# Kernel optimization log

Hardware: AMD Instinct MI355X
Metric: run time of the kernel (lower is better)

Reference implementation:

```python
import jax, jax.numpy as jnp
import numpy as np
from jax.tree_util import tree_map

B, T, D = 2, 4096, 1024
C = 512            # chunk_size
P = 16             # n_persistent
H = 2048           # neural-memory hidden
FFN = 4 * D        # ffn_mult * d_model
LR, BETA, ALPHA = 0.01, 0.9, 0.01   # memory lr / momentum / decay
EPS_LN = 1e-5


def _l2norm(x):
    n = jnp.sqrt(jnp.sum(x * x, axis=-1, keepdims=True))
    return x / jnp.maximum(n, 1e-12)


def _ln(x, g, b):
    m = jnp.mean(x, axis=-1, keepdims=True)
    v = jnp.mean((x - m) ** 2, axis=-1, keepdims=True)
    return (x - m) * jax.lax.rsqrt(v + EPS_LN) * g + b


def _mem_mlp(mem, x):
    h = jax.nn.silu(x @ mem['w0'] + mem['b0'])
    return h @ mem['w1'] + mem['b1']


def setup_inputs() -> dict:
    key = jax.random.key(0)
    ks = iter(jax.random.split(key, 32))
    w = lambda *s: jax.random.normal(next(ks), s, jnp.float32) * 0.02
    return dict(
        x=jax.random.normal(next(ks), (B, T, D), jnp.float32),
        wq_ctx=w(D, D), wq=w(D, D), wk=w(D, D), wv=w(D, D),
        w_attn_out=w(D, D), w_gate=w(D, D),
        gate_g=jnp.ones(D), gate_b=jnp.zeros(D),
        n1_g=jnp.ones(D), n1_b=jnp.zeros(D),
        n2_g=jnp.ones(D), n2_b=jnp.zeros(D),
        ffn_w1=w(D, FFN), ffn_b1=jnp.zeros(FFN),
        ffn_w2=w(FFN, D), ffn_b2=jnp.zeros(D),
        pers=w(P, D),
        mem_w0=w(D, H), mem_b0=jnp.zeros(H),
        mem_w1=w(H, D), mem_b1=jnp.zeros(D),
        mem_wk=w(D, D), mem_wv=w(D, D),
    )


def reference(x, wq_ctx, wq, wk, wv, w_attn_out, w_gate, gate_g, gate_b,
              n1_g, n1_b, n2_g, n2_b, ffn_w1, ffn_b1, ffn_w2, ffn_b2,
              pers, mem_w0, mem_b0, mem_w1, mem_b1, mem_wk, mem_wv):
    Bv, Tv, Dv = x.shape
    n_chunks = Tv // C
    scale = Dv ** 0.5
    S = P + 2 * C   # persistent + retrieved-memory tokens + segment
    # prefix-aware causal mask: i attends to j if j < P (persistent prefix) or j <= i
    ii = jnp.arange(S)[:, None]
    jj = jnp.arange(S)[None, :]
    mask = (jj < P) | (jj <= ii)                      # (S, S)

    mem0 = dict(w0=mem_w0, b0=mem_b0, w1=mem_w1, b1=mem_b1)
    mom0 = tree_map(jnp.zeros_like, mem0)

    def attn(seq):                                    # cosine causal attention, single head
        q = _l2norm(seq @ wq) * scale
        k = _l2norm(seq @ wk)
        v = seq @ wv
        scores = jnp.einsum('bqd,bkd->bqk', q, k)
        scores = jnp.where(mask, scores, -jnp.inf)
        a = jax.nn.softmax(scores, axis=-1)
        return jnp.einsum('bqk,bkd->bqd', a, v) @ w_attn_out

    def step(carry, seg):                             # seg: (B, C, D)
        mem, mom = carry
        h = _mem_mlp(mem, _l2norm(seg @ wq_ctx))      # memory retrieval, (B, C, D)
        aug = jnp.concatenate(
            [jnp.broadcast_to(pers, (Bv, P, Dv)), h, seg], axis=1)  # (B, S, D)
        y_aug = aug + attn(_ln(aug, n1_g, n1_b))
        y_t = y_aug[:, P + C:, :]                     # strip persistent, keep last C

        # surprise-gradient memory update with momentum + decay
        kk = y_t @ mem_wk
        vv = y_t @ mem_wv
        loss = lambda m: 0.5 * jnp.sum((_mem_mlp(m, kk) - vv) ** 2) / (Bv * C)
        g = jax.grad(loss)(mem)
        mom = tree_map(lambda m_, g_: BETA * m_ + g_, mom, g)
        mem = tree_map(lambda p_, m_: (1.0 - ALPHA) * p_ - LR * m_, mem, mom)

        mem_out = _mem_mlp(mem, _l2norm(y_t @ wq_ctx))
        gate = jax.nn.sigmoid(_ln(y_t, gate_g, gate_b) @ w_gate)
        o = y_t * gate + mem_out * (1.0 - gate)
        h2 = _ln(o, n2_g, n2_b)
        o = o + (jax.nn.silu(h2 @ ffn_w1 + ffn_b1) @ ffn_w2 + ffn_b2)
        return (mem, mom), o

    x_chunks = x.reshape(Bv, n_chunks, C, Dv).transpose(1, 0, 2, 3)
    _, outs = jax.lax.scan(step, (mem0, mom0), x_chunks)   # (n_chunks, B, C, D)
    return outs.transpose(1, 0, 2, 3).reshape(Bv, Tv, Dv)
```

## Files before the change

kernel.cpp:

```cpp
#include <hip/hip_runtime.h>

#define DD 1024
#define HH 2048
#define TT 4096
#define CC 512
#define PPc 16
#define SB 1040
#define KA 1088
#define FFd 4096
#define NCH 8

typedef _Float16 f16x8 __attribute__((ext_vector_type(8)));
typedef float f32x4 __attribute__((ext_vector_type(4)));

typedef const __attribute__((address_space(1))) _Float16* gas_t;
typedef __attribute__((address_space(3))) _Float16* las_t;

__device__ __forceinline__ void async_cp16(const _Float16* g, _Float16* l) {
    __builtin_amdgcn_global_load_lds((gas_t)g, (las_t)l, 16, 0, 0);
}

template<int N> __device__ __forceinline__ void waitvm() {
    static_assert(N == 0 || N == 2 || N == 3 || N == 4 || N == 6 || N == 8, "unsupported vmcnt");
    if constexpr (N == 0)      asm volatile("s_waitcnt vmcnt(0)" ::: "memory");
    else if constexpr (N == 2) asm volatile("s_waitcnt vmcnt(2)" ::: "memory");
    else if constexpr (N == 3) asm volatile("s_waitcnt vmcnt(3)" ::: "memory");
    else if constexpr (N == 4) asm volatile("s_waitcnt vmcnt(4)" ::: "memory");
    else if constexpr (N == 6) asm volatile("s_waitcnt vmcnt(6)" ::: "memory");
    else                       asm volatile("s_waitcnt vmcnt(8)" ::: "memory");
}
#define BARRIER() asm volatile("s_barrier" ::: "memory")

struct GP {
    const _Float16* A; long bsA;
    const _Float16* Bt; long bsB;
    const float* bias;
    const float* resid; long ldr, bsR;
    const float* aux;   long ldx, bsX;
    float* Cf; long ldc, bsC;
    _Float16* Ch; long ldh, bsH;
    _Float16* Ct; long ldt, bsT;
    float* Mom;
    float* Cf2;
    float s1, s2;
    int M, N, K, act;
};

template<int BM, int BN>
__global__ __launch_bounds__(256) void gemm16(GP g)
{
    constexpr int WM = BM / 2, WN = BN / 2;
    constexpr int FA = WM / 16, FB = WN / 16;
    constexpr int LA = BM / 32, LB = BN / 32;
    constexpr int LL = LA + LB;
    constexpr int APAN = BM * 64, BPAN = BN * 64;
    constexpr int NB = 3;
    __shared__ _Float16 smem[NB * (APAN + BPAN)];
    const int tid = threadIdx.x;

    const int gx = gridDim.x, gy = gridDim.y;
    const int nwg = gx * gy * (int)gridDim.z;
    const int orig = ((int)blockIdx.z * gy + (int)blockIdx.y) * gx + (int)blockIdx.x;
    const int xcd = orig & 7, loc = orig >> 3;
    const int q8 = nwg >> 3, r8 = nwg & 7;
    const int lid = (xcd < r8 ? xcd * (q8 + 1) : r8 * (q8 + 1) + (xcd - r8) * q8) + loc;
    const int bxi = lid % gx;
    const int rem = lid / gx;
    const int byi = rem % gy;
    const int z = rem / gy;

    const int K = g.K;
    const int m0 = byi * BM, n0 = bxi * BN;
    const _Float16* Ab = g.A + (long)z * g.bsA + (long)m0 * K;
    const _Float16* Bb = g.Bt + (long)z * g.bsB + (long)n0 * K;
    const int wave = tid >> 6, lane = tid & 63;
    const int wr = wave >> 1, wc = wave & 1;
    const int fr = lane & 15, kq = lane >> 4;
    const int srow = tid >> 3;
    const int sc8 = (((tid & 7) ^ (srow & 7)) << 3);
    f32x4 acc[FA][FB] = {};

    auto stage = [&](int q, int kk) {
#pragma unroll
        for (int r = 0; r < LA; ++r)
            async_cp16(Ab + (long)(r * 32 + srow) * K + kk + sc8,
                       &smem[q * APAN + r * 2048 + wave * 512]);
#pragma unroll
        for (int r = 0; r < LB; ++r)
            async_cp16(Bb + (long)(r * 32 + srow) * K + kk + sc8,
                       &smem[NB * APAN + q * BPAN + r * 2048 + wave * 512]);
    };

    const int sl0 = ((kq ^ (fr & 7)) << 3);
    const int sl1 = (((4 + kq) ^ (fr & 7)) << 3);

    auto compute = [&](int q) {
        f16x8 af[2][FA], bf[2][FB];
        const int abase = q * APAN;
#pragma unroll
        for (int i = 0; i < FA; ++i) {
            const int ro = (wr * WM + i * 16 + fr) * 64;
            af[0][i] = *(const f16x8*)&smem[abase + ro + sl0];
            af[1][i] = *(const f16x8*)&smem[abase + ro + sl1];
        }
        const int bbase = NB * APAN + q * BPAN;
#pragma unroll
        for (int j = 0; j < FB; ++j) {
            const int ro = (wc * WN + j * 16 + fr) * 64;
            bf[0][j] = *(const f16x8*)&smem[bbase + ro + sl0];
            bf[1][j] = *(const f16x8*)&smem[bbase + ro + sl1];
        }
        __builtin_amdgcn_s_setprio(1);
#pragma unroll
        for (int h = 0; h < 2; ++h)
#pragma unroll
            for (int i = 0; i < FA; ++i)
#pragma unroll
                for (int j = 0; j < FB; ++j)
                    acc[i][j] = __builtin_amdgcn_mfma_f32_16x16x32_f16(af[h][i], bf[h][j], acc[i][j], 0, 0, 0);
        __builtin_amdgcn_s_setprio(0);
    };

    const int nk = K >> 6;
    stage(0, 0); stage(1, 64);
    int qc = 0, qs = 2;
    for (int t = 0; t < nk; ++t) {
        if (t + 1 < nk) waitvm<LL>(); else waitvm<0>();
        BARRIER();
        if (t + 2 < nk) stage(qs, (t + 2) << 6);
        compute(qc);
        qc = (qc == NB - 1) ? 0 : qc + 1;
        qs = (qs == NB - 1) ? 0 : qs + 1;
    }

#pragma unroll
    for (int i = 0; i < FA; ++i) {
        const int gm0 = m0 + wr * WM + i * 16 + kq * 4;
#pragma unroll
        for (int j = 0; j < FB; ++j) {
            const int gn = n0 + wc * WN + j * 16 + fr;
            if (gn >= g.N) continue;
            if (g.act == 3) {
#pragma unroll
                for (int r = 0; r < 4; ++r) {
                    const int gm = gm0 + r;
                    if (gm >= g.M) continue;
                    const long idx = (long)gm * g.ldc + gn;
                    const float m = 0.9f * g.Mom[idx] + acc[i][j][r];
                    g.Mom[idx] = m;
                    const float v = 0.99f * g.Cf[idx] - 0.01f * m;
                    g.Cf[idx] = v;
                    if (g.Ch) g.Ch[(long)gm * g.ldh + gn] = (_Float16)v;
                    acc[i][j][r] = v;
                }
            } else if (g.act == 4) {
                const int seg = gn >> 10, gl = gn & 1023;
#pragma unroll
                for (int r = 0; r < 4; ++r) {
                    const int gm = gm0 + r;
                    if (gm >= g.M) continue;
                    const float v = acc[i][j][r];
                    if (seg == 0) g.Ch[(long)gm * 1024 + gl] = (_Float16)v;
                    else if (seg == 1) g.Cf[(long)gm * 1024 + gl] = v;
                    else g.Cf2[(long)gm * 1024 + gl] = v;
                }
            } else {
                const float bv = g.bias ? g.bias[gn] : 0.f;
#pragma unroll
                for (int r = 0; r < 4; ++r) {
                    const int gm = gm0 + r;
                    if (gm >= g.M) continue;
                    const float raw = acc[i][j][r] + bv;
                    float av = raw;
                    if (g.act == 1) av = raw / (1.f + __expf(-raw));
                    else if (g.act == 2) {
                        const float a = g.aux[(long)z * g.bsX + (long)gm * g.ldx + gn];
                        const float s = 1.f / (1.f + __expf(-a));
                        av = raw * (s * (1.f + a * (1.f - s)));
                    }
                    float v = g.s1 * av;
                    if (g.resid) v += g.s2 * g.resid[(long)z * g.bsR + (long)gm * g.ldr + gn];
                    if (g.Cf) g.Cf[(long)z * g.bsC + (long)gm * g.ldc + gn] = (g.act == 1) ? raw : v;
                    if (g.Ch) g.Ch[(long)z * g.bsH + (long)gm * g.ldh + gn] = (_Float16)v;
                    acc[i][j][r] = v;
                }
            }
        }
    }

    if (g.Ct && (g.act != 4 || n0 < 1024)) {
        constexpr int TP = BM + 8;
        __syncthreads();
#pragma unroll
        for (int i = 0; i < FA; ++i) {
            const int lm = wr * WM + i * 16 + kq * 4;
#pragma unroll
            for (int j = 0; j < FB; ++j) {
                const int ln = wc * WN + j * 16 + fr;
#pragma unroll
                for (int r = 0; r < 4; ++r)
                    smem[ln * TP + lm + r] = (_Float16)acc[i][j][r];
            }
        }
        __syncthreads();
        constexpr int TPC = 256 / BN;
        constexpr int SEG = BM / TPC;
        const int ln = tid / TPC, part = tid % TPC;
        const int gn = n0 + ln;
        if (gn < g.N) {
            const int gmb = m0 + part * SEG;
            _Float16* dst = g.Ct + (long)z * g.bsT + (long)gn * g.ldt + gmb;
            const _Float16* src = &smem[ln * TP + part * SEG];
#pragma unroll
            for (int gi = 0; gi < SEG / 8; ++gi)
                if (gmb + gi * 8 < g.M)
                    *(uint4*)(dst + gi * 8) = *(const uint4*)(src + gi * 8);
        }
    }
}

__global__ void cvt_k(const float* __restrict__ in, _Float16* __restrict__ out, long n)
{
    long i = ((long)blockIdx.x * 256 + threadIdx.x) * 4;
    if (i >= n) return;
    const float4 v = *(const float4*)(in + i);
    out[i] = (_Float16)v.x; out[i + 1] = (_Float16)v.y;
    out[i + 2] = (_Float16)v.z; out[i + 3] = (_Float16)v.w;
}

__global__ void cvtT_k(const float* __restrict__ in, _Float16* __restrict__ out, int R, int C)
{
    __shared__ _Float16 t[64][65];
    const int c0 = blockIdx.x * 64, r0 = blockIdx.y * 64;
    const int tid = threadIdx.x;
    for (int i = 0; i < 16; ++i) {
        const int lin = i * 256 + tid;
        const int r = lin >> 6, cc = lin & 63;
        t[r][cc] = (_Float16)in[(long)(r0 + r) * C + c0 + cc];
    }
    __syncthreads();
    for (int i = 0; i < 16; ++i) {
        const int lin = i * 256 + tid;
        const int r2 = lin >> 6, c2 = lin & 63;
        out[(long)(c0 + r2) * R + r0 + c2] = t[c2][r2];
    }
}

__global__ void l2n16s_k(const float* __restrict__ in, long ld,
                         _Float16* __restrict__ out, float scale)
{
    const long row = blockIdx.x;
    const float* p = in + row * ld;
    _Float16* q = out + row * DD;
    const int t = threadIdx.x;
    float e0 = p[t], e1 = p[t + 256], e2 = p[t + 512], e3 = p[t + 768];
    __shared__ float rq[256];
    rq[t] = e0 * e0 + e1 * e1 + e2 * e2 + e3 * e3;
    __syncthreads();
    for (int k = 128; k; k >>= 1) { if (t < k) rq[t] += rq[t + k]; __syncthreads(); }
    const float f = scale / fmaxf(sqrtf(rq[0]), 1e-12f);
    q[t] = (_Float16)(e0 * f); q[t + 256] = (_Float16)(e1 * f);
    q[t + 512] = (_Float16)(e2 * f); q[t + 768] = (_Float16)(e3 * f);
}

__global__ void l2qk_k(const float* __restrict__ qk, _Float16* __restrict__ q16,
                       _Float16* __restrict__ k16)
{
    const int blk = blockIdx.x;
    const float* p; _Float16* o; float scale;
    if (blk < 1024) {
        const int b = blk >> 9, r = blk & 511;
        p = qk + (long)(b * SB + PPc + CC + r) * 2048;
        o = q16 + (long)blk * DD; scale = 32.f;
    } else {
        const int row = blk - 1024;
        p = qk + (long)row * 2048 + 1024;
        o = k16 + (long)row * DD; scale = 1.f;
    }
    const int t = threadIdx.x;
    float e0 = p[t], e1 = p[t + 256], e2 = p[t + 512], e3 = p[t + 768];
    __shared__ float rq[256];
    rq[t] = e0 * e0 + e1 * e1 + e2 * e2 + e3 * e3;
    __syncthreads();
    for (int k = 128; k; k >>= 1) { if (t < k) rq[t] += rq[t + k]; __syncthreads(); }
    const float f = scale / fmaxf(sqrtf(rq[0]), 1e-12f);
    o[t] = (_Float16)(e0 * f); o[t + 256] = (_Float16)(e1 * f);
    o[t + 512] = (_Float16)(e2 * f); o[t + 768] = (_Float16)(e3 * f);
}

__global__ void ln16_k(const float* __restrict__ x, const float* __restrict__ g,
                       const float* __restrict__ b, _Float16* __restrict__ o)
{
    const long row = blockIdx.x;
    const float* p = x + row * DD;
    _Float16* q = o + row * DD;
    const int t = threadIdx.x;
    float e0 = p[t], e1 = p[t + 256], e2 = p[t + 512], e3 = p[t + 768];
    __shared__ float rs[256], rq[256];
    rs[t] = e0 + e1 + e2 + e3;
    rq[t] = e0 * e0 + e1 * e1 + e2 * e2 + e3 * e3;
    __syncthreads();
    for (int k = 128; k; k >>= 1) {
        if (t < k) { rs[t] += rs[t + k]; rq[t] += rq[t + k]; }
        __syncthreads();
    }
    const float mean = rs[0] * (1.f / DD);
    const float inv = rsqrtf(rq[0] * (1.f / DD) - mean * mean + 1e-5f);
    q[t]       = (_Float16)((e0 - mean) * inv * g[t]       + b[t]);
    q[t + 256] = (_Float16)((e1 - mean) * inv * g[t + 256] + b[t + 256]);
    q[t + 512] = (_Float16)((e2 - mean) * inv * g[t + 512] + b[t + 512]);
    q[t + 768] = (_Float16)((e3 - mean) * inv * g[t + 768] + b[t + 768]);
}

__global__ void lnaug_k(const float* __restrict__ x, const float* __restrict__ pers,
                        const float* __restrict__ h, const float* __restrict__ g,
                        const float* __restrict__ b, _Float16* __restrict__ out, int c)
{
    const int row = blockIdx.x;
    const int bb = row / SB, i = row % SB;
    const float* p;
    if (i < PPc) p = pers + (long)i * DD;
    else if (i < PPc + CC) p = h + (long)(bb * CC + i - PPc) * DD;
    else p = x + (long)(bb * TT + c * CC + (i - PPc - CC)) * DD;
    _Float16* q = out + (long)row * DD;
    const int t = threadIdx.x;
    float e0 = p[t], e1 = p[t + 256], e2 = p[t + 512], e3 = p[t + 768];
    __shared__ float rs[256], rq[256];
    rs[t] = e0 + e1 + e2 + e3;
    rq[t] = e0 * e0 + e1 * e1 + e2 * e2 + e3 * e3;
    __syncthreads();
    for (int k = 128; k; k >>= 1) {
        if (t < k) { rs[t] += rs[t + k]; rq[t] += rq[t + k]; }
        __syncthreads();
    }
    const float mean = rs[0] * (1.f / DD);
    const float inv = rsqrtf(rq[0] * (1.f / DD) - mean * mean + 1e-5f);
    q[t]       = (_Float16)((e0 - mean) * inv * g[t]       + b[t]);
    q[t + 256] = (_Float16)((e1 - mean) * inv * g[t + 256] + b[t + 256]);
    q[t + 512] = (_Float16)((e2 - mean) * inv * g[t + 512] + b[t + 512]);
    q[t + 768] = (_Float16)((e3 - mean) * inv * g[t + 768] + b[t + 768]);
}

__global__ void softmax16_k(const float* __restrict__ sc, _Float16* __restrict__ pr)
{
    const int blk = blockIdx.x;
    const int r = blk & 511;
    const int i = PPc + CC + r;
    const float* p = sc + (long)blk * SB;
    _Float16* q = pr + (long)blk * KA;
    const int t = threadIdx.x;
    __shared__ float red[256];
    float mx = -3.0e38f;
    for (int j = t; j < SB; j += 256)
        if (j <= i) mx = fmaxf(mx, p[j]);
    red[t] = mx; __syncthreads();
    for (int k = 128; k; k >>= 1) { if (t < k) red[t] = fmaxf(red[t], red[t + k]); __syncthreads(); }
    mx = red[0]; __syncthreads();
    float sum = 0.f;
    for (int j = t; j < SB; j += 256)
        if (j <= i) sum += __expf(p[j] - mx);
    red[t] = sum; __syncthreads();
    for (int k = 128; k; k >>= 1) { if (t < k) red[t] += red[t + k]; __syncthreads(); }
    const float inv = 1.f / red[0];
    for (int j = t; j < KA; j += 256) {
        float e = 0.f;
        if (j < SB && j <= i) e = __expf(p[j] - mx) * inv;
        q[j] = (_Float16)e;
    }
}

__global__ void gateln2_k(const float* __restrict__ yt, const float* __restrict__ gp,
                          const float* __restrict__ mo, const float* __restrict__ g,
                          const float* __restrict__ b, float* __restrict__ OF,
                          _Float16* __restrict__ o16)
{
    const long row = blockIdx.x;
    const int t = threadIdx.x;
    float e[4];
    __shared__ float rs[256], rq[256];
    float ssum = 0.f, qsum = 0.f;
#pragma unroll
    for (int k = 0; k < 4; ++k) {
        const long idx = row * DD + t + k * 256;
        const float s = 1.f / (1.f + __expf(-gp[idx]));
        e[k] = yt[idx] * s + mo[idx] * (1.f - s);
        OF[idx] = e[k];
        ssum += e[k]; qsum += e[k] * e[k];
    }
    rs[t] = ssum; rq[t] = qsum;
    __syncthreads();
    for (int k = 128; k; k >>= 1) {
        if (t < k) { rs[t] += rs[t + k]; rq[t] += rq[t + k]; }
        __syncthreads();
    }
    const float mean = rs[0] * (1.f / DD);
    const float inv = rsqrtf(rq[0] * (1.f / DD) - mean * mean + 1e-5f);
#pragma unroll
    for (int k = 0; k < 4; ++k) {
        const int cc = t + k * 256;
        o16[row * DD + cc] = (_Float16)((e[k] - mean) * inv * g[cc] + b[cc]);
    }
}

__global__ void rowsum2_k(const _Float16* __restrict__ rT, const _Float16* __restrict__ daT,
                          float* __restrict__ db1, float* __restrict__ db0)
{
    const int blk = blockIdx.x;
    const _Float16* p; float* o;
    if (blk < 1024) { p = rT + (long)blk * 1024; o = db1 + blk; }
    else { p = daT + (long)(blk - 1024) * 1024; o = db0 + (blk - 1024); }
    const int t = threadIdx.x;
    __shared__ float red[256];
    red[t] = (float)p[t] + (float)p[t + 256] + (float)p[t + 512] + (float)p[t + 768];
    __syncthreads();
    for (int k = 128; k; k >>= 1) { if (t < k) red[t] += red[t + k]; __syncthreads(); }
    if (t == 0) *o = red[0];
}

__global__ void biasup_k(float* __restrict__ mb0, float* __restrict__ mob0,
                         const float* __restrict__ db0,
                         float* __restrict__ mb1, float* __restrict__ mob1,
                         const float* __restrict__ db1)
{
    const int i = blockIdx.x * 256 + threadIdx.x;
    if (i < HH) {
        const float m = 0.9f * mob0[i] + db0[i];
        mob0[i] = m;
        mb0[i] = 0.99f * mb0[i] - 0.01f * m;
    } else {
        const int j = i - HH;
        if (j < DD) {
            const float m = 0.9f * mob1[j] + db1[j];
            mob1[j] = m;
            mb1[j] = 0.99f * mb1[j] - 0.01f * m;
        }
    }
}

__global__ void zero_k(float* __restrict__ p, long n)
{
    long i = (long)blockIdx.x * 256 + threadIdx.x;
    const long st = (long)gridDim.x * 256;
    for (; i < n; i += st) p[i] = 0.f;
}

extern "C" void kernel_launch(void* const* d_in, const int* in_sizes, int n_in,
                              void* d_out, int out_size, void* d_ws, size_t ws_size,
                              hipStream_t stream)
{
    const float* x          = (const float*)d_in[0];
    const float* wq_ctx     = (const float*)d_in[1];
    const float* wq         = (const float*)d_in[2];
    const float* wk         = (const float*)d_in[3];
    const float* wv         = (const float*)d_in[4];
    const float* w_attn_out = (const float*)d_in[5];
    const float* w_gate     = (const float*)d_in[6];
    const float* gate_g     = (const float*)d_in[7];
    const float* gate_b     = (const float*)d_in[8];
    const float* n1_g       = (const float*)d_in[9];
    const float* n1_b       = (const float*)d_in[10];
    const float* n2_g       = (const float*)d_in[11];
    const float* n2_b       = (const float*)d_in[12];
    const float* ffn_w1     = (const float*)d_in[13];
    const float* ffn_b1     = (const float*)d_in[14];
    const float* ffn_w2     = (const float*)d_in[15];
    const float* ffn_b2     = (const float*)d_in[16];
    const float* pers       = (const float*)d_in[17];
    const float* mem_w0_in  = (const float*)d_in[18];
    const float* mem_b0_in  = (const float*)d_in[19];
    const float* mem_w1_in  = (const float*)d_in[20];
    const float* mem_b1_in  = (const float*)d_in[21];
    const float* mem_wk     = (const float*)d_in[22];
    const float* mem_wv     = (const float*)d_in[23];
    float* out = (float*)d_out;
    (void)in_sizes; (void)n_in; (void)out_size; (void)ws_size;

    char* cur = (char*)d_ws;
    auto allocF = [&](size_t n) { float* p = (float*)cur; cur += n * 4; return p; };
    auto allocH = [&](size_t n) { _Float16* p = (_Float16*)cur; cur += n * 2; return p; };

    float* mw0   = allocF((size_t)DD * HH);
    float* mw1   = allocF((size_t)HH * DD);
    float* mb0   = allocF(HH);
    float* mb1   = allocF(DD);
    float* mom   = allocF((size_t)DD * HH * 2 + HH + DD);
    float* mom_w0 = mom, *mom_w1 = mom + (size_t)DD * HH;
    float* mom_b0 = mom_w1 + (size_t)HH * DD, *mom_b1 = mom_b0 + HH;
    float* F32A  = allocF((size_t)1024 * DD);
    float* F32B  = allocF((size_t)1024 * DD);
    float* F32C  = allocF((size_t)1024 * HH);
    float* F32QK = allocF((size_t)2112 * 2048);
    float* YTF   = allocF((size_t)1024 * DD);
    float* OF    = allocF((size_t)1024 * DD);
    float* db0   = allocF(HH);
    float* db1   = allocF(DD);

    _Float16* x16    = allocH((size_t)2 * TT * DD);
    _Float16* wqcT   = allocH((size_t)DD * DD);
    _Float16* wqkT   = allocH((size_t)2048 * DD);
    _Float16* wvT    = allocH((size_t)DD * DD);
    _Float16* waoT   = allocH((size_t)DD * DD);
    _Float16* wgT    = allocH((size_t)DD * DD);
    _Float16* wmixT  = allocH((size_t)3072 * DD);
    _Float16* f1T    = allocH((size_t)FFd * DD);
    _Float16* f2T    = allocH((size_t)DD * FFd);
    _Float16* w0T    = allocH((size_t)HH * DD);
    _Float16* w1T    = allocH((size_t)DD * HH);
    _Float16* w1p    = allocH((size_t)HH * DD);
    _Float16* xn16   = allocH((size_t)1024 * DD);
    _Float16* h116   = allocH((size_t)1024 * HH);
    _Float16* laug16 = allocH((size_t)2208 * DD);
    _Float16* q16    = allocH((size_t)1024 * DD);
    _Float16* k16    = allocH((size_t)2208 * DD);
    _Float16* vT16   = allocH((size_t)2 * DD * KA);
    _Float16* pr16   = allocH((size_t)2 * 512 * KA);
    _Float16* ao16   = allocH((size_t)1024 * DD);
    _Float16* yt16   = allocH((size_t)1024 * DD);
    _Float16* kk16   = allocH((size_t)1024 * DD);
    _Float16* kkT16  = allocH((size_t)DD * 1024);
    _Float16* hs16   = allocH((size_t)1024 * HH);
    _Float16* hsT16  = allocH((size_t)HH * 1024);
    _Float16* r16    = allocH((size_t)1024 * DD);
    _Float16* rT16   = allocH((size_t)DD * 1024);
    _Float16* da0T   = allocH((size_t)HH * 1024);
    _Float16* qm16   = allocH((size_t)1024 * DD);
    _Float16* a216   = allocH((size_t)1024 * HH);
    _Float16* gl16   = allocH((size_t)1024 * DD);
    _Float16* h216   = allocH((size_t)1024 * DD);
    _Float16* f116   = allocH((size_t)1024 * FFd);

    auto launch = [&](int nz, const GP& g) {
        dim3 grid((g.N + 63) / 64, (g.M + 63) / 64, nz);
        gemm16<64, 64><<<grid, 256, 0, stream>>>(g);
    };

    hipMemcpyAsync(mw0, mem_w0_in, sizeof(float) * DD * HH, hipMemcpyDeviceToDevice, stream);
    hipMemcpyAsync(mw1, mem_w1_in, sizeof(float) * HH * DD, hipMemcpyDeviceToDevice, stream);
    hipMemcpyAsync(mb0, mem_b0_in, sizeof(float) * HH, hipMemcpyDeviceToDevice, stream);
    hipMemcpyAsync(mb1, mem_b1_in, sizeof(float) * DD, hipMemcpyDeviceToDevice, stream);
    zero_k<<<4096, 256, 0, stream>>>(mom, (long)DD * HH * 2 + HH + DD);
    cvt_k<<<(2 * TT * DD) / 1024, 256, 0, stream>>>(x, x16, (long)2 * TT * DD);
    auto T64 = [&](const float* in, _Float16* o, int R, int C) {
        cvtT_k<<<dim3(C / 64, R / 64), 256, 0, stream>>>(in, o, R, C);
    };
    T64(wq_ctx, wqcT, DD, DD);
    T64(wq, wqkT, DD, DD); T64(wk, wqkT + (size_t)1024 * DD, DD, DD);
    T64(wv, wvT, DD, DD); T64(w_attn_out, waoT, DD, DD); T64(w_gate, wgT, DD, DD);
    T64(mem_wk, wmixT, DD, DD); T64(mem_wv, wmixT + (size_t)1024 * DD, DD, DD);
    T64(wq_ctx, wmixT + (size_t)2048 * DD, DD, DD);
    T64(ffn_w1, f1T, DD, FFd); T64(ffn_w2, f2T, FFd, DD);
    T64(mem_w0_in, w0T, DD, HH); T64(mem_w1_in, w1T, HH, DD);
    cvt_k<<<(HH * DD) / 1024, 256, 0, stream>>>(mem_w1_in, w1p, (long)HH * DD);

    for (int c = 0; c < NCH; ++c) {
        GP g;
        g = GP{}; g.A = x16 + (long)c * CC * DD; g.bsA = (long)TT * DD; g.Bt = wqcT;
        g.Cf = F32A; g.ldc = DD; g.bsC = (long)CC * DD;
        g.s1 = 1.f; g.M = CC; g.N = DD; g.K = DD;
        launch(2, g);
        l2n16s_k<<<1024, 256, 0, stream>>>(F32A, DD, xn16, 1.f);
        g = GP{}; g.A = xn16; g.Bt = w0T; g.bias = mb0; g.Ch = h116; g.ldh = HH;
        g.s1 = 1.f; g.M = 1024; g.N = HH; g.K = DD; g.act = 1;
        launch(1, g);
        g = GP{}; g.A = h116; g.Bt = w1T; g.bias = mb1; g.Cf = F32B; g.ldc = DD;
        g.s1 = 1.f; g.M = 1024; g.N = DD; g.K = HH;
        launch(1, g);
        lnaug_k<<<2 * SB, 256, 0, stream>>>(x, pers, F32B, n1_g, n1_b, laug16, c);
        g = GP{}; g.A = laug16; g.Bt = wqkT; g.Cf = F32QK; g.ldc = 2048;
        g.s1 = 1.f; g.M = 2 * SB; g.N = 2048; g.K = DD;
        launch(1, g);
        l2qk_k<<<3104, 256, 0, stream>>>(F32QK, q16, k16);
        g = GP{}; g.A = laug16; g.bsA = (long)SB * DD; g.Bt = wvT;
        g.Ct = vT16; g.ldt = KA; g.bsT = (long)DD * KA;
        g.s1 = 1.f; g.M = SB; g.N = DD; g.K = DD;
        launch(2, g);
        g = GP{}; g.A = q16; g.bsA = (long)512 * DD; g.Bt = k16; g.bsB = (long)SB * DD;
        g.Cf = F32C; g.ldc = SB; g.bsC = (long)512 * SB;
        g.s1 = 1.f; g.M = 512; g.N = SB; g.K = DD;
        launch(2, g);
        softmax16_k<<<1024, 256, 0, stream>>>(F32C, pr16);
        g = GP{}; g.A = pr16; g.bsA = (long)512 * KA; g.Bt = vT16; g.bsB = (long)DD * KA;
        g.Ch = ao16; g.ldh = DD; g.bsH = (long)512 * DD;
        g.s1 = 1.f; g.M = 512; g.N = DD; g.K = KA;
        launch(2, g);
        g = GP{}; g.A = ao16; g.bsA = (long)512 * DD; g.Bt = waoT;
        g.resid = x + (long)c * CC * DD; g.ldr = DD; g.bsR = (long)TT * DD;
        g.Cf = YTF; g.ldc = DD; g.bsC = (long)512 * DD;
        g.Ch = yt16; g.ldh = DD; g.bsH = (long)512 * DD;
        g.s1 = 1.f; g.s2 = 1.f; g.M = 512; g.N = DD; g.K = DD;
        launch(2, g);
        g = GP{}; g.A = yt16; g.Bt = wmixT; g.Ch = kk16; g.Ct = kkT16; g.ldt = 1024;
        g.Cf = F32B; g.Cf2 = F32A;
        g.s1 = 1.f; g.M = 1024; g.N = 3072; g.K = DD; g.act = 4;
        launch(1, g);
        g = GP{}; g.A = kk16; g.Bt = w0T; g.bias = mb0; g.Cf = F32C; g.ldc = HH;
        g.Ch = hs16; g.ldh = HH; g.Ct = hsT16; g.ldt = 1024;
        g.s1 = 1.f; g.M = 1024; g.N = HH; g.K = DD; g.act = 1;
        launch(1, g);
        g = GP{}; g.A = hs16; g.Bt = w1T; g.bias = mb1;
        g.resid = F32B; g.ldr = DD;
        g.Ch = r16; g.ldh = DD; g.Ct = rT16; g.ldt = 1024;
        g.s1 = 1.f / 1024.f; g.s2 = -1.f / 1024.f; g.M = 1024; g.N = DD; g.K = HH;
        launch(1, g);
        g = GP{}; g.A = r16; g.Bt = w1p; g.aux = F32C; g.ldx = HH;
        g.Ct = da0T; g.ldt = 1024;
        g.s1 = 1.f; g.M = 1024; g.N = HH; g.K = DD; g.act = 2;
        launch(1, g);
        rowsum2_k<<<3072, 256, 0, stream>>>(rT16, da0T, db1, db0);
        g = GP{}; g.A = hsT16; g.Bt = rT16; g.Cf = mw1; g.ldc = DD; g.Mom = mom_w1;
        g.Ch = w1p; g.ldh = DD; g.Ct = w1T; g.ldt = HH;
        g.M = HH; g.N = DD; g.K = 1024; g.act = 3;
        launch(1, g);
        g = GP{}; g.A = kkT16; g.Bt = da0T; g.Cf = mw0; g.ldc = HH; g.Mom = mom_w0;
        g.Ct = w0T; g.ldt = DD;
        g.M = DD; g.N = HH; g.K = 1024; g.act = 3;
        launch(1, g);
        biasup_k<<<12, 256, 0, stream>>>(mb0, mom_b0, db0, mb1, mom_b1, db1);
        l2n16s_k<<<1024, 256, 0, stream>>>(F32A, DD, qm16, 1.f);
        g = GP{}; g.A = qm16; g.Bt = w0T; g.bias = mb0; g.Ch = a216; g.ldh = HH;
        g.s1 = 1.f; g.M = 1024; g.N = HH; g.K = DD; g.act = 1;
        launch(1, g);
        g = GP{}; g.A = a216; g.Bt = w1T; g.bias = mb1; g.Cf = F32B; g.ldc = DD;
        g.s1 = 1.f; g.M = 1024; g.N = DD; g.K = HH;
        launch(1, g);
        ln16_k<<<1024, 256, 0, stream>>>(YTF, gate_g, gate_b, gl16);
        g = GP{}; g.A = gl16; g.Bt = wgT; g.Cf = F32C; g.ldc = DD;
        g.s1 = 1.f; g.M = 1024; g.N = DD; g.K = DD;
        launch(1, g);
        gateln2_k<<<1024, 256, 0, stream>>>(YTF, F32C, F32B, n2_g, n2_b, OF, h216);
        g = GP{}; g.A = h216; g.Bt = f1T; g.bias = ffn_b1; g.Ch = f116; g.ldh = FFd;
        g.s1 = 1.f; g.M = 1024; g.N = FFd; g.K = DD; g.act = 1;
        launch(1, g);
        g = GP{}; g.A = f116; g.bsA = (long)512 * FFd; g.Bt = f2T; g.bias = ffn_b2;
        g.resid = OF; g.ldr = DD; g.bsR = (long)512 * DD;
        g.Cf = out + (long)c * CC * DD; g.ldc = DD; g.bsC = (long)TT * DD;
        g.s1 = 1.f; g.s2 = 1.f; g.M = 512; g.N = DD; g.K = FFd;
        launch(2, g);
    }
}
```

Before: 3.152 ms.

## Batch independent GEMMs into grouped launches, fuse tail kernels, hoist query projection

Adds a grouped GEMM kernel that runs two independent GEMMs in one launch: V-projection with QK scores, the two weight-gradient updates, and memory-output with gate projection. This fills the GPU better and removes launch gaps. It also merges the bias rowsum/update, the l2norm of the query and the gate LayerNorm into one kernel. The x@wq_ctx projection plus l2norm, which does not depend on the memory state, is moved out of the chunk loop and done once over the whole sequence. The price is a larger xn16 buffer and a more complex scheduling of blocks.

```diff
diff --git a/kernel.cpp b/kernel.cpp
--- a/kernel.cpp
+++ b/kernel.cpp
@@ -47,7 +47,7 @@
 };
 
 template<int BM, int BN>
-__global__ __launch_bounds__(256) void gemm16(GP g)
+__device__ __forceinline__ void gemm_body(const GP& g, int bxi, int byi, int z)
 {
     constexpr int WM = BM / 2, WN = BN / 2;
     constexpr int FA = WM / 16, FB = WN / 16;
@@ -57,17 +57,6 @@
     constexpr int NB = 3;
     __shared__ _Float16 smem[NB * (APAN + BPAN)];
     const int tid = threadIdx.x;
-
-    const int gx = gridDim.x, gy = gridDim.y;
-    const int nwg = gx * gy * (int)gridDim.z;
-    const int orig = ((int)blockIdx.z * gy + (int)blockIdx.y) * gx + (int)blockIdx.x;
-    const int xcd = orig & 7, loc = orig >> 3;
-    const int q8 = nwg >> 3, r8 = nwg & 7;
-    const int lid = (xcd < r8 ? xcd * (q8 + 1) : r8 * (q8 + 1) + (xcd - r8) * q8) + loc;
-    const int bxi = lid % gx;
-    const int rem = lid / gx;
-    const int byi = rem % gy;
-    const int z = rem / gy;
 
     const int K = g.K;
     const int m0 = byi * BM, n0 = bxi * BN;
@@ -219,6 +208,37 @@
     }
 }
 
+template<int BM, int BN>
+__global__ __launch_bounds__(256) void gemm16(GP g)
+{
+    const int gx = gridDim.x, gy = gridDim.y;
+    const int nwg = gx * gy * (int)gridDim.z;
+    const int orig = ((int)blockIdx.z * gy + (int)blockIdx.y) * gx + (int)blockIdx.x;
+    const int xcd = orig & 7, loc = orig >> 3;
+    const int q8 = nwg >> 3, r8 = nwg & 7;
+    const int lid = (xcd < r8 ? xcd * (q8 + 1) : r8 * (q8 + 1) + (xcd - r8) * q8) + loc;
+    const int bxi = lid % gx;
+    const int rem = lid / gx;
+    gemm_body<BM, BN>(g, bxi, rem % gy, rem / gy);
+}
+
+template<int BM, int BN>
+__global__ __launch_bounds__(256) void gemm16p(GP g0, int nb0, int gx0, int gy0,
+                                               GP g1, int gx1, int gy1)
+{
+    const int nwg = gridDim.x;
+    const int orig = blockIdx.x;
+    const int xcd = orig & 7, loc = orig >> 3;
+    const int q8 = nwg >> 3, r8 = nwg & 7;
+    const int lid = (xcd < r8 ? xcd * (q8 + 1) : r8 * (q8 + 1) + (xcd - r8) * q8) + loc;
+    const GP* gp; int l, gx, gy;
+    if (lid < nb0) { gp = &g0; l = lid;       gx = gx0; gy = gy0; }
+    else           { gp = &g1; l = lid - nb0; gx = gx1; gy = gy1; }
+    const int bxi = l % gx;
+    const int r = l / gx;
+    gemm_body<BM, BN>(*gp, bxi, r % gy, r / gy);
+}
+
 __global__ void cvt_k(const float* __restrict__ in, _Float16* __restrict__ out, long n)
 {
     long i = ((long)blockIdx.x * 256 + threadIdx.x) * 4;
@@ -286,30 +306,6 @@
     const float f = scale / fmaxf(sqrtf(rq[0]), 1e-12f);
     o[t] = (_Float16)(e0 * f); o[t + 256] = (_Float16)(e1 * f);
     o[t + 512] = (_Float16)(e2 * f); o[t + 768] = (_Float16)(e3 * f);
-}
-
-__global__ void ln16_k(const float* __restrict__ x, const float* __restrict__ g,
-                       const float* __restrict__ b, _Float16* __restrict__ o)
-{
-    const long row = blockIdx.x;
-    const float* p = x + row * DD;
-    _Float16* q = o + row * DD;
-    const int t = threadIdx.x;
-    float e0 = p[t], e1 = p[t + 256], e2 = p[t + 512], e3 = p[t + 768];
-    __shared__ float rs[256], rq[256];
-    rs[t] = e0 + e1 + e2 + e3;
-    rq[t] = e0 * e0 + e1 * e1 + e2 * e2 + e3 * e3;
-    __syncthreads();
-    for (int k = 128; k; k >>= 1) {
-        if (t < k) { rs[t] += rs[t + k]; rq[t] += rq[t + k]; }
-        __syncthreads();
-    }
-    const float mean = rs[0] * (1.f / DD);
-    const float inv = rsqrtf(rq[0] * (1.f / DD) - mean * mean + 1e-5f);
-    q[t]       = (_Float16)((e0 - mean) * inv * g[t]       + b[t]);
-    q[t + 256] = (_Float16)((e1 - mean) * inv * g[t + 256] + b[t + 256]);
-    q[t + 512] = (_Float16)((e2 - mean) * inv * g[t + 512] + b[t + 512]);
-    q[t + 768] = (_Float16)((e3 - mean) * inv * g[t + 768] + b[t + 768]);
 }
 
 __global__ void lnaug_k(const float* __restrict__ x, const float* __restrict__ pers,
@@ -402,38 +398,64 @@
     }
 }
 
-__global__ void rowsum2_k(const _Float16* __restrict__ rT, const _Float16* __restrict__ daT,
-                          float* __restrict__ db1, float* __restrict__ db0)
+__global__ void tailfuse_k(const _Float16* __restrict__ rT, const _Float16* __restrict__ daT,
+                           float* __restrict__ mb0, float* __restrict__ mob0,
+                           float* __restrict__ mb1, float* __restrict__ mob1,
+                           const float* __restrict__ qmp, _Float16* __restrict__ qm16,
+                           const float* __restrict__ ytf, const float* __restrict__ gg,
+                           const float* __restrict__ gb, _Float16* __restrict__ gl)
 {
     const int blk = blockIdx.x;
-    const _Float16* p; float* o;
-    if (blk < 1024) { p = rT + (long)blk * 1024; o = db1 + blk; }
-    else { p = daT + (long)(blk - 1024) * 1024; o = db0 + (blk - 1024); }
     const int t = threadIdx.x;
-    __shared__ float red[256];
-    red[t] = (float)p[t] + (float)p[t + 256] + (float)p[t + 512] + (float)p[t + 768];
-    __syncthreads();
-    for (int k = 128; k; k >>= 1) { if (t < k) red[t] += red[t + k]; __syncthreads(); }
-    if (t == 0) *o = red[0];
-}
-
-__global__ void biasup_k(float* __restrict__ mb0, float* __restrict__ mob0,
-                         const float* __restrict__ db0,
-                         float* __restrict__ mb1, float* __restrict__ mob1,
-                         const float* __restrict__ db1)
-{
-    const int i = blockIdx.x * 256 + threadIdx.x;
-    if (i < HH) {
-        const float m = 0.9f * mob0[i] + db0[i];
-        mob0[i] = m;
-        mb0[i] = 0.99f * mb0[i] - 0.01f * m;
+    __shared__ float rs[256], rq[256];
+    if (blk < 3072) {
+        const _Float16* p = (blk < 1024) ? rT + (long)blk * 1024
+                                         : daT + (long)(blk - 1024) * 1024;
+        rs[t] = (float)p[t] + (float)p[t + 256] + (float)p[t + 512] + (float)p[t + 768];
+        __syncthreads();
+        for (int k = 128; k; k >>= 1) { if (t < k) rs[t] += rs[t + k]; __syncthreads(); }
+        if (t == 0) {
+            const float d = rs[0];
+            if (blk < 1024) {
+                const float m = 0.9f * mob1[blk] + d;
+                mob1[blk] = m;
+                mb1[blk] = 0.99f * mb1[blk] - 0.01f * m;
+            } else {
+                const int j = blk - 1024;
+                const float m = 0.9f * mob0[j] + d;
+                mob0[j] = m;
+                mb0[j] = 0.99f * mb0[j] - 0.01f * m;
+            }
+        }
+    } else if (blk < 4096) {
+        const long row = blk - 3072;
+        const float* p = qmp + row * DD;
+        _Float16* q = qm16 + row * DD;
+        float e0 = p[t], e1 = p[t + 256], e2 = p[t + 512], e3 = p[t + 768];
+        rq[t] = e0 * e0 + e1 * e1 + e2 * e2 + e3 * e3;
+        __syncthreads();
+        for (int k = 128; k; k >>= 1) { if (t < k) rq[t] += rq[t + k]; __syncthreads(); }
+        const float f = 1.f / fmaxf(sqrtf(rq[0]), 1e-12f);
+        q[t] = (_Float16)(e0 * f); q[t + 256] = (_Float16)(e1 * f);
+        q[t + 512] = (_Float16)(e2 * f); q[t + 768] = (_Float16)(e3 * f);
     } else {
-        const int j = i - HH;
-        if (j < DD) {
-            const float m = 0.9f * mob1[j] + db1[j];
-            mob1[j] = m;
-            mb1[j] = 0.99f * mb1[j] - 0.01f * m;
+        const long row = blk - 4096;
+        const float* p = ytf + row * DD;
+        _Float16* q = gl + row * DD;
+        float e0 = p[t], e1 = p[t + 256], e2 = p[t + 512], e3 = p[t + 768];
+        rs[t] = e0 + e1 + e2 + e3;
+        rq[t] = e0 * e0 + e1 * e1 + e2 * e2 + e3 * e3;
+        __syncthreads();
+        for (int k = 128; k; k >>= 1) {
+            if (t < k) { rs[t] += rs[t + k]; rq[t] += rq[t + k]; }
+            __syncthreads();
         }
+        const float mean = rs[0] * (1.f / DD);
+        const float inv = rsqrtf(rq[0] * (1.f / DD) - mean * mean + 1e-5f);
+        q[t]       = (_Float16)((e0 - mean) * inv * gg[t]       + gb[t]);
+        q[t + 256] = (_Float16)((e1 - mean) * inv * gg[t + 256] + gb[t + 256]);
+        q[t + 512] = (_Float16)((e2 - mean) * inv * gg[t + 512] + gb[t + 512]);
+        q[t + 768] = (_Float16)((e3 - mean) * inv * gg[t + 768] + gb[t + 768]);
     }
 }
 
@@ -494,6 +516,7 @@
     float* OF    = allocF((size_t)1024 * DD);
     float* db0   = allocF(HH);
     float* db1   = allocF(DD);
+    (void)db0; (void)db1;
 
     _Float16* x16    = allocH((size_t)2 * TT * DD);
     _Float16* wqcT   = allocH((size_t)DD * DD);
@@ -507,7 +530,7 @@
     _Float16* w0T    = allocH((size_t)HH * DD);
     _Float16* w1T    = allocH((size_t)DD * HH);
     _Float16* w1p    = allocH((size_t)HH * DD);
-    _Float16* xn16   = allocH((size_t)1024 * DD);
+    _Float16* xn16   = allocH((size_t)2 * TT * DD);
     _Float16* h116   = allocH((size_t)1024 * HH);
     _Float16* laug16 = allocH((size_t)2208 * DD);
     _Float16* q16    = allocH((size_t)1024 * DD);
@@ -529,9 +552,17 @@
     _Float16* h216   = allocH((size_t)1024 * DD);
     _Float16* f116   = allocH((size_t)1024 * FFd);
 
+    float* XN = F32C;
+
     auto launch = [&](int nz, const GP& g) {
         dim3 grid((g.N + 63) / 64, (g.M + 63) / 64, nz);
         gemm16<64, 64><<<grid, 256, 0, stream>>>(g);
+    };
+    auto launchp = [&](int nz0, const GP& g0, int nz1, const GP& g1) {
+        const int gx0 = (g0.N + 63) / 64, gy0 = (g0.M + 63) / 64;
+        const int gx1 = (g1.N + 63) / 64, gy1 = (g1.M + 63) / 64;
+        const int nb0 = gx0 * gy0 * nz0, nb1 = gx1 * gy1 * nz1;
+        gemm16p<64, 64><<<nb0 + nb1, 256, 0, stream>>>(g0, nb0, gx0, gy0, g1, gx1, gy1);
     };
 
     hipMemcpyAsync(mw0, mem_w0_in, sizeof(float) * DD * HH, hipMemcpyDeviceToDevice, stream);
@@ -552,16 +583,19 @@
     T64(mem_w0_in, w0T, DD, HH); T64(mem_w1_in, w1T, HH, DD);
     cvt_k<<<(HH * DD) / 1024, 256, 0, stream>>>(mem_w1_in, w1p, (long)HH * DD);
 
+    {
+        GP g{}; g.A = x16; g.Bt = wqcT; g.Cf = XN; g.ldc = DD;
+        g.s1 = 1.f; g.M = 2 * TT; g.N = DD; g.K = DD;
+        launch(1, g);
+        l2n16s_k<<<2 * TT, 256, 0, stream>>>(XN, DD, xn16, 1.f);
+    }
+
     for (int c = 0; c < NCH; ++c) {
         GP g;
-        g = GP{}; g.A = x16 + (long)c * CC * DD; g.bsA = (long)TT * DD; g.Bt = wqcT;
-        g.Cf = F32A; g.ldc = DD; g.bsC = (long)CC * DD;
-        g.s1 = 1.f; g.M = CC; g.N = DD; g.K = DD;
+        g = GP{}; g.A = xn16 + (long)c * CC * DD; g.bsA = (long)TT * DD;
+        g.Bt = w0T; g.bias = mb0; g.Ch = h116; g.ldh = HH; g.bsH = (long)CC * HH;
+        g.s1 = 1.f; g.M = CC; g.N = HH; g.K = DD; g.act = 1;
         launch(2, g);
-        l2n16s_k<<<1024, 256, 0, stream>>>(F32A, DD, xn16, 1.f);
-        g = GP{}; g.A = xn16; g.Bt = w0T; g.bias = mb0; g.Ch = h116; g.ldh = HH;
-        g.s1 = 1.f; g.M = 1024; g.N = HH; g.K = DD; g.act = 1;
-        launch(1, g);
         g = GP{}; g.A = h116; g.Bt = w1T; g.bias = mb1; g.Cf = F32B; g.ldc = DD;
         g.s1 = 1.f; g.M = 1024; g.N = DD; g.K = HH;
         launch(1, g);
@@ -570,14 +604,13 @@
         g.s1 = 1.f; g.M = 2 * SB; g.N = 2048; g.K = DD;
         launch(1, g);
         l2qk_k<<<3104, 256, 0, stream>>>(F32QK, q16, k16);
-        g = GP{}; g.A = laug16; g.bsA = (long)SB * DD; g.Bt = wvT;
-        g.Ct = vT16; g.ldt = KA; g.bsT = (long)DD * KA;
-        g.s1 = 1.f; g.M = SB; g.N = DD; g.K = DD;
-        launch(2, g);
-        g = GP{}; g.A = q16; g.bsA = (long)512 * DD; g.Bt = k16; g.bsB = (long)SB * DD;
-        g.Cf = F32C; g.ldc = SB; g.bsC = (long)512 * SB;
-        g.s1 = 1.f; g.M = 512; g.N = SB; g.K = DD;
-        launch(2, g);
+        GP g4{}; g4.A = laug16; g4.bsA = (long)SB * DD; g4.Bt = wvT;
+        g4.Ct = vT16; g4.ldt = KA; g4.bsT = (long)DD * KA;
+        g4.s1 = 1.f; g4.M = SB; g4.N = DD; g4.K = DD;
+        GP g5{}; g5.A = q16; g5.bsA = (long)512 * DD; g5.Bt = k16; g5.bsB = (long)SB * DD;
+        g5.Cf = F32C; g5.ldc = SB; g5.bsC = (long)512 * SB;
+        g5.s1 = 1.f; g5.M = 512; g5.N = SB; g5.K = DD;
+        launchp(2, g4, 2, g5);
         softmax16_k<<<1024, 256, 0, stream>>>(F32C, pr16);
         g = GP{}; g.A = pr16; g.bsA = (long)512 * KA; g.Bt = vT16; g.bsB = (long)DD * KA;
         g.Ch = ao16; g.ldh = DD; g.bsH = (long)512 * DD;
@@ -606,27 +639,23 @@
         g.Ct = da0T; g.ldt = 1024;
         g.s1 = 1.f; g.M = 1024; g.N = HH; g.K = DD; g.act = 2;
         launch(1, g);
-        rowsum2_k<<<3072, 256, 0, stream>>>(rT16, da0T, db1, db0);
-        g = GP{}; g.A = hsT16; g.Bt = rT16; g.Cf = mw1; g.ldc = DD; g.Mom = mom_w1;
-        g.Ch = w1p; g.ldh = DD; g.Ct = w1T; g.ldt = HH;
-        g.M = HH; g.N = DD; g.K = 1024; g.act = 3;
-        launch(1, g);
-        g = GP{}; g.A = kkT16; g.Bt = da0T; g.Cf = mw0; g.ldc = HH; g.Mom = mom_w0;
-        g.Ct = w0T; g.ldt = DD;
-        g.M = DD; g.N = HH; g.K = 1024; g.act = 3;
-        launch(1, g);
-        biasup_k<<<12, 256, 0, stream>>>(mb0, mom_b0, db0, mb1, mom_b1, db1);
-        l2n16s_k<<<1024, 256, 0, stream>>>(F32A, DD, qm16, 1.f);
+        tailfuse_k<<<5120, 256, 0, stream>>>(rT16, da0T, mb0, mom_b0, mb1, mom_b1,
+                                             F32A, qm16, YTF, gate_g, gate_b, gl16);
+        GP ga{}; ga.A = hsT16; ga.Bt = rT16; ga.Cf = mw1; ga.ldc = DD; ga.Mom = mom_w1;
+        ga.Ch = w1p; ga.ldh = DD; ga.Ct = w1T; ga.ldt = HH;
+        ga.M = HH; ga.N = DD; ga.K = 1024; ga.act = 3;
+        GP gb{}; gb.A = kkT16; gb.Bt = da0T; gb.Cf = mw0; gb.ldc = HH; gb.Mom = mom_w0;
+        gb.Ct = w0T; gb.ldt = DD;
+        gb.M = DD; gb.N = HH; gb.K = 1024; gb.act = 3;
+        launchp(1, ga, 1, gb);
         g = GP{}; g.A = qm16; g.Bt = w0T; g.bias = mb0; g.Ch = a216; g.ldh = HH;
         g.s1 = 1.f; g.M = 1024; g.N = HH; g.K = DD; g.act = 1;
         launch(1, g);
-        g = GP{}; g.A = a216; g.Bt = w1T; g.bias = mb1; g.Cf = F32B; g.ldc = DD;
-        g.s1 = 1.f; g.M = 1024; g.N = DD; g.K = HH;
-        launch(1, g);
-        ln16_k<<<1024, 256, 0, stream>>>(YTF, gate_g, gate_b, gl16);
-        g = GP{}; g.A = gl16; g.Bt = wgT; g.Cf = F32C; g.ldc = DD;
-        g.s1 = 1.f; g.M = 1024; g.N = DD; g.K = DD;
-        launch(1, g);
+        GP gc{}; gc.A = a216; gc.Bt = w1T; gc.bias = mb1; gc.Cf = F32B; gc.ldc = DD;
+        gc.s1 = 1.f; gc.M = 1024; gc.N = DD; gc.K = HH;
+        GP gd{}; gd.A = gl16; gd.Bt = wgT; gd.Cf = F32C; gd.ldc = DD;
+        gd.s1 = 1.f; gd.M = 1024; gd.N = DD; gd.K = DD;
+        launchp(1, gc, 1, gd);
         gateln2_k<<<1024, 256, 0, stream>>>(YTF, F32C, F32B, n2_g, n2_b, OF, h216);
         g = GP{}; g.A = h216; g.Bt = f1T; g.bias = ffn_b1; g.Ch = f116; g.ldh = FFd;
         g.s1 = 1.f; g.M = 1024; g.N = FFd; g.K = DD; g.act = 1;
```

Result: slower. 3.557 ms (+12.8%).
